# Performance work log

Measured on AMD Instinct MI355X. Metric: run time of the kernel, lower is better.

Reference implementation:

```python
import jax, jax.numpy as jnp
import numpy as np

D = 512
MOMENTUM = 0.99
NEG_INF = -1.0e9


def setup_inputs() -> dict:
    key = jax.random.key(0)
    ks = jax.random.split(key, 16)
    B, Lq, Lk = 16, 1024, 1024
    s = 0.02
    inp = {
        "uncond_q": jax.random.normal(ks[0], (B, D), jnp.float32),
        "q": jax.random.normal(ks[1], (B, Lq, D), jnp.float32),
        "k": jax.random.normal(ks[2], (B, Lk, D), jnp.float32),
        "v": jax.random.normal(ks[3], (B, Lk, D), jnp.float32),
        "src_key_padding_mask": jax.random.randint(ks[4], (B, Lk), 0, 2) > 0,
        "fallback_score": jnp.zeros((1,), jnp.float32),
        # parameters (torch Linear: y = x @ W.T + b)
        "Wv": jax.random.normal(ks[5], (D, D), jnp.float32) * s,
        "bv": jnp.zeros((D,), jnp.float32),
        "Wf": jax.random.normal(ks[6], (D, D), jnp.float32) * s,
        "bf": jnp.zeros((D,), jnp.float32),
        "W1": jax.random.normal(ks[7], (D, D), jnp.float32) * s,
        "b1": jnp.zeros((D,), jnp.float32),
        "W2": jax.random.normal(ks[8], (D // 2, D), jnp.float32) * s,
        "b2": jnp.zeros((D // 2,), jnp.float32),
        "W3": jax.random.normal(ks[9], (1, D // 2), jnp.float32) * s,
        "b3": jnp.zeros((1,), jnp.float32),
    }
    return inp


def _scorer(x, W1, b1, W2, b2, W3, b3):
    h = jax.nn.relu(x @ W1.T + b1)
    h = jax.nn.relu(h @ W2.T + b2)
    return jnp.tanh(h @ W3.T + b3)


def reference(uncond_q, q, k, v, src_key_padding_mask, fallback_score,
              Wv, bv, Wf, bf, W1, b1, W2, b2, W3, b3):
    B, Lq, _ = q.shape
    v_p = v @ Wv.T + bv                                  # [B,Lk,D]
    default_values = (uncond_q @ Wf.T + bf)[:, None, :]  # [B,1,D]

    scores = jnp.einsum('bqd,bkd->bqk', q, k) / jnp.sqrt(jnp.float32(D))

    # EMA fallback-score update (training mode), detached from grads
    bmax = jax.lax.stop_gradient(scores.max())
    bmin = jax.lax.stop_gradient(scores.min())
    fb = MOMENTUM * fallback_score[0] + (1.0 - MOMENTUM) * (bmax + bmin) / 2.0

    scores = jnp.where(src_key_padding_mask[:, None, :], NEG_INF, scores)
    fb_col = jnp.broadcast_to(fb, (B, Lq, 1))
    scores = jnp.concatenate([scores, fb_col], axis=-1)   # [B,Lq,Lk+1]
    weights = jax.nn.softmax(scores, axis=-1)

    v_padded = jnp.concatenate([v_p, default_values], axis=1)  # [B,Lk+1,D]
    out = jnp.einsum('bqk,bkd->bqd', weights, v_padded)

    return (_scorer(out, W1, b1, W2, b2, W3, b3),
            _scorer(default_values, W1, b1, W2, b2, W3, b3))
```

## Files before the change

kernel.cpp:

```cpp
#include <hip/hip_runtime.h>

typedef _Float16 f16;
typedef f16  f16x8 __attribute__((ext_vector_type(8)));
typedef f16  f16x4 __attribute__((ext_vector_type(4)));
typedef float f32x4 __attribute__((ext_vector_type(4)));

__device__ __forceinline__ void gld_lds16(const f16* g, void* l) {
  __builtin_amdgcn_global_load_lds((const __attribute__((address_space(1))) void*)g,
                                   (__attribute__((address_space(3))) void*)l,
                                   16, 0, 0);
}

enum { EPI_SCORES = 0, EPI_RELU = 2, EPI_OUT = 3, EPI_BIASR = 4 };

template<int EPI, bool XMAP>
__global__ __launch_bounds__(256)
void gemm_bt(const f16* __restrict__ A, const f16* __restrict__ B, void* __restrict__ C,
             int lda, int ldb, int ldc, int K,
             long long sA, long long sB, long long sC,
             const float* __restrict__ bias, float scale,
             float* __restrict__ mmarr, int nmm,
             const float* __restrict__ wfb, const float* __restrict__ dvv,
             int nx, int nbz)
{
  __shared__ __align__(16) f16 As[3][128][32];
  __shared__ __align__(16) f16 Bs[3][128][32];
  const int tid  = threadIdx.x;
  const int lane = tid & 63;
  const int w    = tid >> 6;
  const int wm   = w >> 1, wn = w & 1;

  const int lin = blockIdx.x;
  int bz, bj;
  if constexpr (XMAP) {
    const int xcd = lin & 7, rest = lin >> 3;
    const int grp = rest / nbz;
    bj = rest - grp * nbz;
    bz = xcd + (grp << 3);
  } else {
    bz = lin / nbz; bj = lin - bz * nbz;
  }
  const int m0 = (bj / nx) * 128, n0 = (bj % nx) * 128;
  const f16* Ab = A + (size_t)bz * sA + (size_t)m0 * lda;
  const f16* Bb = B + (size_t)bz * sB + (size_t)n0 * ldb;

  f32x4 acc[4][4] = {};
  const int nsteps = K >> 5;

#define STAGE(bufb, ks)                                                              \
  {                                                                                  \
    const int k0_ = (ks) << 5;                                                       \
    _Pragma("unroll")                                                                \
    for (int i = 0; i < 2; ++i) {                                                    \
      const int ci = i * 256 + tid;                                                  \
      const int r  = ci >> 2;                                                        \
      const int sg = (ci & 3) ^ ((r >> 1) & 3);                                      \
      gld_lds16(Ab + (size_t)r * lda + k0_ + sg * 8,                                 \
                (char*)As + (bufb) + (size_t)(i * 256 + w * 64) * 16);               \
      gld_lds16(Bb + (size_t)r * ldb + k0_ + sg * 8,                                 \
                (char*)Bs + (bufb) + (size_t)(i * 256 + w * 64) * 16);               \
    }                                                                                \
  }

  STAGE(0, 0)
  STAGE(8192, 1)

  const int elemoff = (((lane >> 4) ^ ((lane >> 1) & 3)) << 3);

  int cur = 0;
  for (int t = 0; t < nsteps; ++t) {
    if (t + 1 < nsteps) asm volatile("s_waitcnt vmcnt(4)" ::: "memory");
    else                asm volatile("s_waitcnt vmcnt(0)" ::: "memory");
    __builtin_amdgcn_s_barrier();
    __builtin_amdgcn_sched_barrier(0);
    int st = cur + 2; if (st >= 3) st -= 3;
    if (t + 2 < nsteps) STAGE(st * 8192, t + 2)
    f16x8 af[4], bfr[4];
#pragma unroll
    for (int m = 0; m < 4; ++m)
      af[m] = *(const f16x8*)&As[cur][wm * 64 + m * 16 + (lane & 15)][elemoff];
#pragma unroll
    for (int n = 0; n < 4; ++n)
      bfr[n] = *(const f16x8*)&Bs[cur][wn * 64 + n * 16 + (lane & 15)][elemoff];
    __builtin_amdgcn_s_setprio(1);
#pragma unroll
    for (int m = 0; m < 4; ++m)
#pragma unroll
      for (int n = 0; n < 4; ++n)
        acc[m][n] = __builtin_amdgcn_mfma_f32_16x16x32_f16(af[m], bfr[n], acc[m][n], 0, 0, 0);
    __builtin_amdgcn_s_setprio(0);
    cur = (cur + 1 == 3) ? 0 : cur + 1;
  }
#undef STAGE

  const int col_l = lane & 15;
  const int row_l = (lane >> 4) << 2;

  {
    f16* Ch = (f16*)C + (size_t)bz * sC + (size_t)m0 * ldc + n0;
#pragma unroll
    for (int m = 0; m < 4; ++m)
#pragma unroll
      for (int n = 0; n < 4; ++n)
#pragma unroll
        for (int r = 0; r < 4; ++r) {
          const int rr = wm * 64 + m * 16 + row_l + r;
          const int cc = wn * 64 + n * 16 + col_l;
          float val = acc[m][n][r];
          if constexpr (EPI == EPI_RELU) { val += bias[n0 + cc]; val = fmaxf(val, 0.0f); }
          if constexpr (EPI == EPI_BIASR) val += bias[m0 + rr];
          if constexpr (EPI == EPI_OUT)
            val += wfb[bz * 1024 + m0 + rr] * dvv[bz * 512 + n0 + cc];
          Ch[(size_t)rr * ldc + cc] = (f16)val;
        }
  }
  (void)scale; (void)mmarr; (void)nmm;
}

__global__ __launch_bounds__(512, 2)
void gemm256_scores(const f16* __restrict__ A, const f16* __restrict__ B, f16* __restrict__ C,
                    float scale, float* __restrict__ mmarr)
{
  __shared__ __align__(16) f16 As[3][256][32];
  __shared__ __align__(16) f16 Bs[3][256][32];
  __shared__ float redm[8], redn[8];
  const int tid  = threadIdx.x;
  const int lane = tid & 63;
  const int w    = tid >> 6;
  const int wm   = w >> 2, wn = w & 3;
  const int lin  = blockIdx.x;
  const int xcd = lin & 7, rest = lin >> 3;
  const int bj  = rest & 15;
  const int bz  = xcd + ((rest >> 4) << 3);
  const int m0 = (bj >> 2) * 256, n0 = (bj & 3) * 256;
  const f16* Ab = A + (size_t)bz * 524288 + (size_t)m0 * 512;
  const f16* Bb = B + (size_t)bz * 524288 + (size_t)n0 * 512;

  f32x4 acc[8][4] = {};

#define STAGE2(bufb, ks)                                                             \
  {                                                                                  \
    const int k0_ = (ks) << 5;                                                       \
    _Pragma("unroll")                                                                \
    for (int i = 0; i < 2; ++i) {                                                    \
      const int ci = i * 512 + tid;                                                  \
      const int r  = ci >> 2;                                                        \
      const int sg = (ci & 3) ^ ((r >> 1) & 3);                                      \
      gld_lds16(Ab + (size_t)r * 512 + k0_ + sg * 8,                                 \
                (char*)As + (bufb) + (size_t)(i * 512 + w * 64) * 16);               \
      gld_lds16(Bb + (size_t)r * 512 + k0_ + sg * 8,                                 \
                (char*)Bs + (bufb) + (size_t)(i * 512 + w * 64) * 16);               \
    }                                                                                \
  }

  STAGE2(0, 0)
  STAGE2(16384, 1)

  const int elemoff = (((lane >> 4) ^ ((lane >> 1) & 3)) << 3);

  int cur = 0;
  for (int t = 0; t < 16; ++t) {
    if (t + 1 < 16) asm volatile("s_waitcnt vmcnt(4)" ::: "memory");
    else            asm volatile("s_waitcnt vmcnt(0)" ::: "memory");
    __builtin_amdgcn_s_barrier();
    __builtin_amdgcn_sched_barrier(0);
    int st = cur + 2; if (st >= 3) st -= 3;
    if (t + 2 < 16) STAGE2(st * 16384, t + 2)
    f16x8 af[8], bfr[4];
#pragma unroll
    for (int m = 0; m < 8; ++m)
      af[m] = *(const f16x8*)&As[cur][wm * 128 + m * 16 + (lane & 15)][elemoff];
#pragma unroll
    for (int n = 0; n < 4; ++n)
      bfr[n] = *(const f16x8*)&Bs[cur][wn * 64 + n * 16 + (lane & 15)][elemoff];
    __builtin_amdgcn_s_setprio(1);
#pragma unroll
    for (int m = 0; m < 8; ++m)
#pragma unroll
      for (int n = 0; n < 4; ++n)
        acc[m][n] = __builtin_amdgcn_mfma_f32_16x16x32_f16(af[m], bfr[n], acc[m][n], 0, 0, 0);
    __builtin_amdgcn_s_setprio(0);
    cur = (cur + 1 == 3) ? 0 : cur + 1;
  }
#undef STAGE2

  const int col_l = lane & 15;
  const int row_l = (lane >> 4) << 2;
  f16* Ch = C + (size_t)bz * 1048576 + (size_t)m0 * 1024 + n0;
  float lmax = -3.402823466e38f, lmin = 3.402823466e38f;
#pragma unroll
  for (int m = 0; m < 8; ++m)
#pragma unroll
    for (int n = 0; n < 4; ++n)
#pragma unroll
      for (int r = 0; r < 4; ++r) {
        float val = acc[m][n][r] * scale;
        lmax = fmaxf(lmax, val); lmin = fminf(lmin, val);
        Ch[(size_t)(wm * 128 + m * 16 + row_l + r) * 1024 + (wn * 64 + n * 16 + col_l)] = (f16)val;
      }
#pragma unroll
  for (int off = 32; off >= 1; off >>= 1) {
    lmax = fmaxf(lmax, __shfl_xor(lmax, off));
    lmin = fminf(lmin, __shfl_xor(lmin, off));
  }
  if (lane == 0) { redm[w] = lmax; redn[w] = lmin; }
  __syncthreads();
  if (tid == 0) {
    float gm = redm[0], gn = redn[0];
#pragma unroll
    for (int i = 1; i < 8; ++i) { gm = fmaxf(gm, redm[i]); gn = fminf(gn, redn[i]); }
    mmarr[lin] = gm; mmarr[256 + lin] = gn;
  }
}

__global__ __launch_bounds__(256)
void reduce_mm(const float* __restrict__ mmarr, int n,
               const float* __restrict__ fallback, float* __restrict__ fbv)
{
  __shared__ float rm[4], rn[4];
  const int lane = threadIdx.x & 63, w = threadIdx.x >> 6;
  float mx = -3.402823466e38f, mn = 3.402823466e38f;
  for (int i = threadIdx.x; i < n; i += 256) {
    mx = fmaxf(mx, mmarr[i]);
    mn = fminf(mn, mmarr[n + i]);
  }
#pragma unroll
  for (int off = 32; off >= 1; off >>= 1) {
    mx = fmaxf(mx, __shfl_xor(mx, off));
    mn = fminf(mn, __shfl_xor(mn, off));
  }
  if (lane == 0) { rm[w] = mx; rn[w] = mn; }
  __syncthreads();
  if (threadIdx.x == 0) {
    float gmax = fmaxf(fmaxf(rm[0], rm[1]), fmaxf(rm[2], rm[3]));
    float gmin = fminf(fminf(rn[0], rn[1]), fminf(rn[2], rn[3]));
    fbv[0] = 0.99f * fallback[0] + 0.005f * (gmax + gmin);
  }
}

__global__ __launch_bounds__(256)
void conv3_k(const float* __restrict__ a, const float* __restrict__ b,
             const float* __restrict__ c,
             f16* __restrict__ oa, f16* __restrict__ ob, f16* __restrict__ oc,
             int n4each)
{
  int i = blockIdx.x * 256 + threadIdx.x;
  int seg = i / n4each;
  int j = i - seg * n4each;
  const float* src = (seg == 0) ? a : ((seg == 1) ? b : c);
  f16* dst = (seg == 0) ? oa : ((seg == 1) ? ob : oc);
  float4 v = *(const float4*)(src + (size_t)j * 4);
  f16x4 o = { (f16)v.x, (f16)v.y, (f16)v.z, (f16)v.w };
  *(f16x4*)(dst + (size_t)j * 4) = o;
}

__global__ __launch_bounds__(256)
void convw_k(const float* __restrict__ wv, const float* __restrict__ w1,
             const float* __restrict__ w2,
             f16* __restrict__ owv, f16* __restrict__ ow1, f16* __restrict__ ow2)
{
  int i = blockIdx.x * 256 + threadIdx.x;
  const float* src; f16* dst; int j;
  if (i < 65536)       { src = wv; dst = owv; j = i; }
  else if (i < 131072) { src = w1; dst = ow1; j = i - 65536; }
  else                 { src = w2; dst = ow2; j = i - 131072; }
  float4 v = *(const float4*)(src + (size_t)j * 4);
  f16x4 o = { (f16)v.x, (f16)v.y, (f16)v.z, (f16)v.w };
  *(f16x4*)(dst + (size_t)j * 4) = o;
}

__global__ void init_count(const unsigned char* __restrict__ mask, unsigned* __restrict__ mm)
{
  __shared__ int red[256];
  int c = 0;
  for (int i = threadIdx.x; i < 16384; i += 256) c += (mask[i] != 0) ? 1 : 0;
  red[threadIdx.x] = c;
  __syncthreads();
  for (int s = 128; s > 0; s >>= 1) {
    if (threadIdx.x < s) red[threadIdx.x] += red[threadIdx.x + s];
    __syncthreads();
  }
  if (threadIdx.x == 0) mm[0] = (unsigned)red[0];
}

__global__ __launch_bounds__(256)
void softmax_rows(const f16* __restrict__ scores, const void* __restrict__ maskp,
                  const float* __restrict__ fbv, const unsigned* __restrict__ mm,
                  f16* __restrict__ Wt, float* __restrict__ wfb)
{
  __shared__ float red[8];
  const int row  = blockIdx.x;
  const int b    = row >> 10;
  const int tid  = threadIdx.x;
  const int lane = tid & 63, w = tid >> 6;
  const float fb = fbv[0];
  const unsigned mode = (mm[0] > 5000u) ? 1u : 0u;
  const f16* s = scores + (size_t)row * 1024;
  const int k0 = tid * 4;
  f16x4 sv = *(const f16x4*)(s + k0);
  float x[4];
  if (mode) {
    const unsigned char* m8 = (const unsigned char*)maskp + b * 1024 + k0;
    x[0] = m8[0] ? -1e9f : (float)sv[0];  x[1] = m8[1] ? -1e9f : (float)sv[1];
    x[2] = m8[2] ? -1e9f : (float)sv[2];  x[3] = m8[3] ? -1e9f : (float)sv[3];
  } else {
    const int* mi = (const int*)maskp + b * 1024 + k0;
    x[0] = mi[0] ? -1e9f : (float)sv[0];  x[1] = mi[1] ? -1e9f : (float)sv[1];
    x[2] = mi[2] ? -1e9f : (float)sv[2];  x[3] = mi[3] ? -1e9f : (float)sv[3];
  }
  float mx = fmaxf(fmaxf(x[0], x[1]), fmaxf(x[2], x[3]));
#pragma unroll
  for (int off = 32; off >= 1; off >>= 1) mx = fmaxf(mx, __shfl_xor(mx, off));
  if (lane == 0) red[w] = mx;
  __syncthreads();
  mx = fmaxf(fmaxf(fmaxf(red[0], red[1]), fmaxf(red[2], red[3])), fb);
  float e0 = expf(x[0] - mx), e1 = expf(x[1] - mx), e2 = expf(x[2] - mx), e3 = expf(x[3] - mx);
  float sum = (e0 + e1) + (e2 + e3);
#pragma unroll
  for (int off = 32; off >= 1; off >>= 1) sum += __shfl_xor(sum, off);
  if (lane == 0) red[4 + w] = sum;
  __syncthreads();
  float efb = expf(fb - mx);
  float Z = ((red[4] + red[5]) + (red[6] + red[7])) + efb;
  float inv = 1.0f / Z;
  f16x4 o = { (f16)(e0 * inv), (f16)(e1 * inv), (f16)(e2 * inv), (f16)(e3 * inv) };
  *(f16x4*)&Wt[(size_t)row * 1024 + k0] = o;
  if (tid == 0) wfb[row] = efb * inv;
}

template<int IN, int ACT>
__global__ __launch_bounds__(256)
void fc_wave(const float* __restrict__ X, const float* __restrict__ W,
             const float* __restrict__ bias, float* __restrict__ Y, int OutN)
{
  const int gw   = (blockIdx.x * 256 + threadIdx.x) >> 6;
  const int lane = threadIdx.x & 63;
  const int b = gw / OutN, j = gw - b * OutN;
  const float* x  = X + (size_t)b * IN;
  const float* wr = W + (size_t)j * IN;
  float s = 0.f;
  if constexpr (IN == 512) {
    const int o = lane * 8;
    float4 x0 = *(const float4*)(x + o),  x1 = *(const float4*)(x + o + 4);
    float4 w0 = *(const float4*)(wr + o), w1 = *(const float4*)(wr + o + 4);
    s = x0.x*w0.x + x0.y*w0.y + x0.z*w0.z + x0.w*w0.w
      + x1.x*w1.x + x1.y*w1.y + x1.z*w1.z + x1.w*w1.w;
  } else {
    const int o = lane * 4;
    float4 x0 = *(const float4*)(x + o);
    float4 w0 = *(const float4*)(wr + o);
    s = x0.x*w0.x + x0.y*w0.y + x0.z*w0.z + x0.w*w0.w;
  }
#pragma unroll
  for (int off = 32; off >= 1; off >>= 1) s += __shfl_xor(s, off);
  if (lane == 0) {
    float val = s + bias[ACT == 2 ? 0 : j];
    if constexpr (ACT == 1) val = fmaxf(val, 0.f);
    if constexpr (ACT == 2) val = tanhf(val);
    Y[gw] = val;
  }
}

__global__ __launch_bounds__(256)
void y_kernel(const f16* __restrict__ h2, const float* __restrict__ W3,
              const float* __restrict__ b3, float* __restrict__ outp)
{
  int row = blockIdx.x * 16 + (threadIdx.x >> 4);
  int l   = threadIdx.x & 15;
  const f16* h = h2 + (size_t)row * 256 + l * 16;
  float s = 0.f;
#pragma unroll
  for (int j = 0; j < 16; ++j) s += (float)h[j] * W3[l * 16 + j];
#pragma unroll
  for (int off = 1; off < 16; off <<= 1) s += __shfl_xor(s, off);
  if (l == 0) outp[row] = tanhf(s + b3[0]);
}

extern "C" void kernel_launch(void* const* d_in, const int* in_sizes, int n_in,
                              void* d_out, int out_size, void* d_ws, size_t ws_size,
                              hipStream_t stream) {
  const float* uq       = (const float*)d_in[0];
  const float* q        = (const float*)d_in[1];
  const float* kk       = (const float*)d_in[2];
  const float* v        = (const float*)d_in[3];
  const void*  mask     = d_in[4];
  const float* fallback = (const float*)d_in[5];
  const float* Wv = (const float*)d_in[6];
  const float* bv = (const float*)d_in[7];
  const float* Wf = (const float*)d_in[8];
  const float* bf = (const float*)d_in[9];
  const float* W1 = (const float*)d_in[10];
  const float* b1 = (const float*)d_in[11];
  const float* W2 = (const float*)d_in[12];
  const float* b2 = (const float*)d_in[13];
  const float* W3 = (const float*)d_in[14];
  const float* b3 = (const float*)d_in[15];
  float* outp = (float*)d_out;

  char* ws = (char*)d_ws;
  const size_t MB = 1ull << 20;
  f16*  scores = (f16*)ws;
  f16*  h1b  = (f16*)ws;
  f16*  h2b  = (f16*)(ws + 16 * MB);
  f16*  vpt  = (f16*)(ws + 32 * MB);
  f16*  outb = (f16*)(ws + 48 * MB);
  f16*  q16  = (f16*)(ws + 64 * MB);
  f16*  wts  = (f16*)(ws + 64 * MB);
  f16*  k16  = (f16*)(ws + 80 * MB);
  f16*  v16  = (f16*)(ws + 96 * MB);
  char* cst  = ws + 112 * MB;
  f16*  Wv16 = (f16*)(cst);
  f16*  W116 = (f16*)(cst + 512 * 1024);
  f16*  W216 = (f16*)(cst + 1024 * 1024);
  float* dv   = (float*)(cst + 1280 * 1024);
  float* wfb  = (float*)(cst + 1312 * 1024);
  float* h1d  = (float*)(cst + 1376 * 1024);
  float* h2d  = (float*)(cst + 1408 * 1024);
  unsigned* mm = (unsigned*)(cst + 1424 * 1024);
  float* fbv   = (float*)(cst + 1428 * 1024);
  float* mmarr = (float*)(cst + 1432 * 1024);

  init_count<<<1, 256, 0, stream>>>((const unsigned char*)mask, mm);

  conv3_k<<<24576, 256, 0, stream>>>(q, kk, v, q16, k16, v16, 2097152);
  convw_k<<<640, 256, 0, stream>>>(Wv, W1, W2, Wv16, W116, W216);

  fc_wave<512, 0><<<2048, 256, 0, stream>>>(uq, Wf, bf, dv, 512);

  gemm256_scores<<<256, 512, 0, stream>>>(q16, k16, scores, 0.04419417382415922f, mmarr);

  reduce_mm<<<1, 256, 0, stream>>>(mmarr, 256, fallback, fbv);

  softmax_rows<<<16384, 256, 0, stream>>>(scores, mask, fbv, mm, wts, wfb);

  gemm_bt<EPI_BIASR, true><<<512, 256, 0, stream>>>(
      Wv16, v16, vpt, 512, 512, 1024, 512,
      0LL, 524288LL, 524288LL,
      bv, 1.f, nullptr, 0, nullptr, nullptr, 8, 32);

  gemm_bt<EPI_OUT, true><<<512, 256, 0, stream>>>(
      wts, vpt, outb, 1024, 1024, 512, 1024,
      1048576LL, 524288LL, 524288LL,
      nullptr, 1.f, nullptr, 0, wfb, dv, 4, 32);

  gemm_bt<EPI_RELU, false><<<512, 256, 0, stream>>>(
      outb, W116, h1b, 512, 512, 512, 512, 0LL, 0LL, 0LL,
      b1, 1.f, nullptr, 0, nullptr, nullptr, 4, 512);

  gemm_bt<EPI_RELU, false><<<256, 256, 0, stream>>>(
      h1b, W216, h2b, 512, 512, 256, 512, 0LL, 0LL, 0LL,
      b2, 1.f, nullptr, 0, nullptr, nullptr, 2, 256);

  y_kernel<<<1024, 256, 0, stream>>>(h2b, W3, b3, outp);

  fc_wave<512, 1><<<2048, 256, 0, stream>>>(dv, W1, b1, h1d, 512);
  fc_wave<512, 1><<<1024, 256, 0, stream>>>(h1d, W2, b2, h2d, 256);
  fc_wave<256, 2><<<4, 256, 0, stream>>>(h2d, W3, b3, outp + 16384, 1);

  (void)in_sizes; (void)n_in; (void)out_size; (void)ws_size;
}
```

Before: 181.5 us.

## Use 256x128 tiles with 512 threads for the Vproj, PV and first scorer GEMMs

```diff
diff --git a/kernel.cpp b/kernel.cpp
--- a/kernel.cpp
+++ b/kernel.cpp
@@ -115,6 +115,109 @@
         }
   }
   (void)scale; (void)mmarr; (void)nmm;
+}
+
+template<int EPI, bool XMAP>
+__global__ __launch_bounds__(512, 2)
+void gemm_bt2(const f16* __restrict__ A, const f16* __restrict__ B, void* __restrict__ C,
+              int lda, int ldb, int ldc, int K,
+              long long sA, long long sB, long long sC,
+              const float* __restrict__ bias,
+              const float* __restrict__ wfb, const float* __restrict__ dvv,
+              int nx, int nbz)
+{
+  __shared__ __align__(16) f16 As[3][256][32];
+  __shared__ __align__(16) f16 Bs[3][128][32];
+  const int tid  = threadIdx.x;
+  const int lane = tid & 63;
+  const int w    = tid >> 6;
+  const int wm   = w >> 1, wn = w & 1;
+
+  const int lin = blockIdx.x;
+  int bz, bj;
+  if constexpr (XMAP) {
+    const int xcd = lin & 7, rest = lin >> 3;
+    const int grp = rest / nbz;
+    bj = rest - grp * nbz;
+    bz = xcd + (grp << 3);
+  } else {
+    bz = lin / nbz; bj = lin - bz * nbz;
+  }
+  const int m0 = (bj / nx) * 256, n0 = (bj % nx) * 128;
+  const f16* Ab = A + (size_t)bz * sA + (size_t)m0 * lda;
+  const f16* Bb = B + (size_t)bz * sB + (size_t)n0 * ldb;
+
+  f32x4 acc[4][4] = {};
+  const int nsteps = K >> 5;
+
+#define STAGE3(bufb, ks)                                                             \
+  {                                                                                  \
+    const int k0_ = (ks) << 5;                                                       \
+    _Pragma("unroll")                                                                \
+    for (int i = 0; i < 2; ++i) {                                                    \
+      const int ci = i * 512 + tid;                                                  \
+      const int r  = ci >> 2;                                                        \
+      const int sg = (ci & 3) ^ ((r >> 1) & 3);                                      \
+      gld_lds16(Ab + (size_t)r * lda + k0_ + sg * 8,                                 \
+                (char*)As + (size_t)(bufb) * 16384 + (size_t)(i * 512 + w * 64) * 16); \
+    }                                                                                \
+    {                                                                                \
+      const int r  = tid >> 2;                                                       \
+      const int sg = (tid & 3) ^ ((r >> 1) & 3);                                     \
+      gld_lds16(Bb + (size_t)r * ldb + k0_ + sg * 8,                                 \
+                (char*)Bs + (size_t)(bufb) * 8192 + (size_t)(w * 64) * 16);          \
+    }                                                                                \
+  }
+
+  STAGE3(0, 0)
+  STAGE3(1, 1)
+
+  const int elemoff = (((lane >> 4) ^ ((lane >> 1) & 3)) << 3);
+
+  int cur = 0;
+  for (int t = 0; t < nsteps; ++t) {
+    if (t + 1 < nsteps) asm volatile("s_waitcnt vmcnt(3)" ::: "memory");
+    else                asm volatile("s_waitcnt vmcnt(0)" ::: "memory");
+    __builtin_amdgcn_s_barrier();
+    __builtin_amdgcn_sched_barrier(0);
+    int st = cur + 2; if (st >= 3) st -= 3;
+    if (t + 2 < nsteps) STAGE3(st, t + 2)
+    f16x8 af[4], bfr[4];
+#pragma unroll
+    for (int m = 0; m < 4; ++m)
+      af[m] = *(const f16x8*)&As[cur][wm * 64 + m * 16 + (lane & 15)][elemoff];
+#pragma unroll
+    for (int n = 0; n < 4; ++n)
+      bfr[n] = *(const f16x8*)&Bs[cur][wn * 64 + n * 16 + (lane & 15)][elemoff];
+    __builtin_amdgcn_s_setprio(1);
+#pragma unroll
+    for (int m = 0; m < 4; ++m)
+#pragma unroll
+      for (int n = 0; n < 4; ++n)
+        acc[m][n] = __builtin_amdgcn_mfma_f32_16x16x32_f16(af[m], bfr[n], acc[m][n], 0, 0, 0);
+    __builtin_amdgcn_s_setprio(0);
+    cur = (cur + 1 == 3) ? 0 : cur + 1;
+  }
+#undef STAGE3
+
+  const int col_l = lane & 15;
+  const int row_l = (lane >> 4) << 2;
+  f16* Ch = (f16*)C + (size_t)bz * sC + (size_t)m0 * ldc + n0;
+#pragma unroll
+  for (int m = 0; m < 4; ++m)
+#pragma unroll
+    for (int n = 0; n < 4; ++n)
+#pragma unroll
+      for (int r = 0; r < 4; ++r) {
+        const int rr = wm * 64 + m * 16 + row_l + r;
+        const int cc = wn * 64 + n * 16 + col_l;
+        float val = acc[m][n][r];
+        if constexpr (EPI == EPI_RELU) { val += bias[n0 + cc]; val = fmaxf(val, 0.0f); }
+        if constexpr (EPI == EPI_BIASR) val += bias[m0 + rr];
+        if constexpr (EPI == EPI_OUT)
+          val += wfb[bz * 1024 + m0 + rr] * dvv[bz * 512 + n0 + cc];
+        Ch[(size_t)rr * ldc + cc] = (f16)val;
+      }
 }
 
 __global__ __launch_bounds__(512, 2)
@@ -433,19 +536,19 @@
 
   softmax_rows<<<16384, 256, 0, stream>>>(scores, mask, fbv, mm, wts, wfb);
 
-  gemm_bt<EPI_BIASR, true><<<512, 256, 0, stream>>>(
+  gemm_bt2<EPI_BIASR, true><<<256, 512, 0, stream>>>(
       Wv16, v16, vpt, 512, 512, 1024, 512,
       0LL, 524288LL, 524288LL,
-      bv, 1.f, nullptr, 0, nullptr, nullptr, 8, 32);
-
-  gemm_bt<EPI_OUT, true><<<512, 256, 0, stream>>>(
+      bv, nullptr, nullptr, 8, 16);
+
+  gemm_bt2<EPI_OUT, true><<<256, 512, 0, stream>>>(
       wts, vpt, outb, 1024, 1024, 512, 1024,
       1048576LL, 524288LL, 524288LL,
-      nullptr, 1.f, nullptr, 0, wfb, dv, 4, 32);
-
-  gemm_bt<EPI_RELU, false><<<512, 256, 0, stream>>>(
+      nullptr, wfb, dv, 4, 16);
+
+  gemm_bt2<EPI_RELU, false><<<256, 512, 0, stream>>>(
       outb, W116, h1b, 512, 512, 512, 512, 0LL, 0LL, 0LL,
-      b1, 1.f, nullptr, 0, nullptr, nullptr, 4, 512);
+      b1, nullptr, nullptr, 4, 256);
 
   gemm_bt<EPI_RELU, false><<<256, 256, 0, stream>>>(
       h1b, W216, h2b, 512, 512, 256, 512, 0LL, 0LL, 0LL,
```

After: 190.3 us. +4.8%, slower.
